# Optimization experiments

Hardware: AMD Instinct MI355X
Metric: run time of the kernel (lower is better)

## Reference

```python
import jax, jax.numpy as jnp
import numpy as np

TAU = 0.6  # BGK relaxation time (>= 0.5 per __post_init__ stability check)
# D2Q9 lattice: velocities, weights, opposite-direction indices
E = np.array([[0, 0], [1, 0], [0, 1], [-1, 0], [0, -1],
              [1, 1], [-1, 1], [-1, -1], [1, -1]], dtype=np.int32)
W = np.array([4.0 / 9] + [1.0 / 9] * 4 + [1.0 / 36] * 4, dtype=np.float32)
OPP = np.array([0, 3, 4, 1, 2, 7, 8, 5, 6], dtype=np.int32)


def setup_inputs() -> dict:
    key = jax.random.key(0)
    k1, k2, k3 = jax.random.split(key, 3)
    nx, ny = 2048, 2048
    f = jax.random.uniform(k1, (nx, ny, 9), dtype=jnp.float32)  # positive populations
    rho = jnp.sum(f, axis=-1)                                    # consistent density
    u = 0.05 * jax.random.normal(k2, (nx, ny, 2), dtype=jnp.float32)  # low-Ma velocity
    obstacle_mask = jax.random.uniform(k3, (nx, ny)) < 0.01      # sparse solid cells
    return {"f": f, "rho": rho, "u": u, "obstacle_mask": obstacle_mask}


def _equilibrium(rho, u):
    # feq_i = w_i * rho * (1 + 3 e.u + 4.5 (e.u)^2 - 1.5 u.u)
    e = jnp.asarray(E, jnp.float32)
    w = jnp.asarray(W)
    eu = jnp.einsum('xyd,qd->xyq', u, e)              # [nx, ny, 9]
    usq = jnp.sum(u * u, axis=-1, keepdims=True)       # [nx, ny, 1]
    return w * rho[..., None] * (1.0 + 3.0 * eu + 4.5 * eu * eu - 1.5 * usq)


def reference(f, rho, u, obstacle_mask):
    # --- collide (BGK) ---
    feq = _equilibrium(rho, u)
    f_star = f - (f - feq) / TAU
    # --- stream: roll each direction by its lattice velocity (lattice not shifted) ---
    f_new = jnp.stack(
        [jnp.roll(f_star[..., i], shift=(int(E[i, 0]), int(E[i, 1])), axis=(0, 1))
         for i in range(9)],
        axis=-1,
    )
    # --- obstacle bounce-back: solid cells reflect post-collision populations ---
    f_bb = f_star[..., jnp.asarray(OPP)]
    f_new = jnp.where(obstacle_mask[..., None], f_bb, f_new)
    # --- lift macro fields from post-stream distributions ---
    rho_new = jnp.sum(f_new, axis=-1)
    e = jnp.asarray(E, jnp.float32)
    u_new = jnp.einsum('xyq,qd->xyd', f_new, e) / rho_new[..., None]
    # pack (f_new [..9], rho_new [..1], u_new [..2]) -> [nx, ny, 12]
    return jnp.concatenate([f_new, rho_new[..., None], u_new], axis=-1)
```

## Files before the change

### kernel.cpp

```cpp
#include <hip/hip_runtime.h>


#define NX 2048
#define NY 2048
#define WRAP 2047
#define TR 8
#define TC 64
#define NT 512
#define HR (TR + 2)
#define HC (TC + 2)
#define HCELLS (HR * HC)
#define HELEMS (HCELLS * 9)
#define CACHEF (HCELLS * 4)
#define FP_ITERS 12
#define STAGE_WORDS (NT * 13)

typedef float floatx4 __attribute__((ext_vector_type(4)));

__global__ __launch_bounds__(NT) void lbm_step_kernel(
    const float* __restrict__ f,
    const float* __restrict__ rho,
    const float* __restrict__ u,
    const int*   __restrict__ mask,
    float*       __restrict__ out)
{
    __shared__ float lds[HELEMS + CACHEF];
    floatx4* cache = reinterpret_cast<floatx4*>(lds + HELEMS);

    const int tid = threadIdx.x;
    const int y0 = blockIdx.x * TC;
    const int x0 = blockIdx.y * TR;
    const float INV_TAU = 1.0f / 0.6f;

    const float2* __restrict__ u2 = reinterpret_cast<const float2*>(u);

    float fpre[FP_ITERS];
    #pragma unroll
    for (int it = 0; it < FP_ITERS; ++it) {
        const int k = tid + it * NT;
        if (k < HELEMS) {
            const unsigned cell = (unsigned)k / 9u;
            const int i  = k - (int)cell * 9;
            const unsigned hr = cell / (unsigned)HC;
            const int hc = (int)cell - (int)hr * HC;
            const int xr = (x0 - 1 + (int)hr) & WRAP;
            const int yc = (y0 - 1 + hc) & WRAP;
            const int g  = xr * NY + yc;
            fpre[it] = f[(size_t)g * 9 + i];
        }
    }

    const int r = tid >> 6;
    const int c = tid & 63;
    const int cidx = (x0 + r) * NY + (y0 + c);
    const int m = mask[cidx];

    for (int k = tid; k < HCELLS; k += NT) {
        const unsigned hr = (unsigned)k / (unsigned)HC;
        const int hc = k - (int)hr * HC;
        const int xr = (x0 - 1 + (int)hr) & WRAP;
        const int yc = (y0 - 1 + hc) & WRAP;
        const int g  = xr * NY + yc;
        const float  rn = rho[g];
        const float2 uv = u2[g];
        const float usq = uv.x * uv.x + uv.y * uv.y;
        floatx4 v;
        v.x = rn - 1.5f * rn * usq;
        v.y = 3.0f * rn * uv.x;
        v.z = 3.0f * rn * uv.y;
        v.w = __builtin_amdgcn_rcpf(rn + rn);
        cache[k] = v;
    }
    __syncthreads();

    #pragma unroll
    for (int it = 0; it < FP_ITERS; ++it) {
        const int k = tid + it * NT;
        if (k < HELEMS) {
            const unsigned cell = (unsigned)k / 9u;
            const int i  = k - (int)cell * 9;
            const floatx4 v = cache[cell];
            const float exf = (float)((int)((0x20919u >> (2 * i)) & 3u) - 1);
            const float eyf = (float)((int)((0x2865u  >> (2 * i)) & 3u) - 1);
            const float wi  = (i == 0) ? (4.0f / 9.0f)
                                       : ((i < 5) ? (1.0f / 9.0f) : (1.0f / 36.0f));
            const float t   = v.y * exf + v.z * eyf;
            const float feq = wi * (v.x + t + t * t * v.w);
            const float fi  = fpre[it];
            lds[k] = fi - (fi - feq) * INV_TAU;
        }
    }
    __syncthreads();

    const int ex9[9]  = {0, 1, 0, -1, 0, 1, -1, -1, 1};
    const int ey9[9]  = {0, 0, 1, 0, -1, 1, 1, -1, -1};
    const int opp9[9] = {0, 3, 4, 1, 2, 7, 8, 5, 6};

    float fn[9];
    #pragma unroll
    for (int i = 0; i < 9; ++i) {
        const int lsrc = (r + 1 - ex9[i]) * HC + (c + 1 - ey9[i]);
        fn[i] = lds[lsrc * 9 + i];
    }
    if (m) {
        const int lc = ((r + 1) * HC + (c + 1)) * 9;
        #pragma unroll
        for (int i = 0; i < 9; ++i) fn[i] = lds[lc + opp9[i]];
    }

    const float rhon = fn[0] + fn[1] + fn[2] + fn[3] + fn[4]
                     + fn[5] + fn[6] + fn[7] + fn[8];
    const float irho = __builtin_amdgcn_rcpf(rhon);
    const float uxn = (fn[1] - fn[3] + fn[5] - fn[6] - fn[7] + fn[8]) * irho;
    const float uyn = (fn[2] - fn[4] + fn[5] + fn[6] - fn[7] - fn[8]) * irho;

    __syncthreads();

    {
        const int b = tid * 13;
        #pragma unroll
        for (int i = 0; i < 9; ++i) lds[b + i] = fn[i];
        lds[b + 9]  = rhon;
        lds[b + 10] = uxn;
        lds[b + 11] = uyn;
    }
    __syncthreads();

    #pragma unroll
    for (int it = 0; it < 3; ++it) {
        const int k4 = tid + it * NT;
        const unsigned r2  = (unsigned)k4 / 192u;
        const int      rem = k4 - (int)r2 * 192;
        const unsigned cc  = (unsigned)rem / 3u;
        const int      q   = rem - (int)cc * 3;
        const int lbase = (int)r2 * (TC * 13) + (int)cc * 13 + q * 4;
        floatx4 v;
        v.x = lds[lbase + 0];
        v.y = lds[lbase + 1];
        v.z = lds[lbase + 2];
        v.w = lds[lbase + 3];
        const size_t obase = ((size_t)(x0 + (int)r2) * NY + y0) * 12 + (size_t)rem * 4;
        __builtin_nontemporal_store(v, reinterpret_cast<floatx4*>(out + obase));
    }
}

extern "C" void kernel_launch(void* const* d_in, const int* in_sizes, int n_in,
                              void* d_out, int out_size, void* d_ws, size_t ws_size,
                              hipStream_t stream) {
    const float* f    = (const float*)d_in[0];
    const float* rho  = (const float*)d_in[1];
    const float* u    = (const float*)d_in[2];
    const int*   mask = (const int*)d_in[3];
    float* out = (float*)d_out;

    dim3 block(NT, 1, 1);
    dim3 grid(NY / TC, NX / TR, 1);
    lbm_step_kernel<<<grid, block, 0, stream>>>(f, rho, u, mask, out);
}
```

Baseline: 349.4 us.

## Vectorize halo loads with row-contiguous LDS layout and per-cell collision

Reorganizes the LDS tile so each halo row stores its 64 interior cells contiguously, followed by the two wrap-around edge cells. Interior rows can then be loaded from global memory with 16-byte vector loads instead of scalar per-element gathers. Collision moves from per-element to per-cell, computing all nine equilibria from one rho/u read with shared subexpressions, and the separate rho/u cache array is dropped. Launch bounds now request 8 waves per EU. The cost is more register pressure per thread and special-case column indexing for the edge cells.

```diff
diff --git a/kernel.cpp b/kernel.cpp
--- a/kernel.cpp
+++ b/kernel.cpp
@@ -7,105 +7,136 @@
 #define TR 8
 #define TC 64
 #define NT 512
-#define HR (TR + 2)
-#define HC (TC + 2)
-#define HCELLS (HR * HC)
-#define HELEMS (HCELLS * 9)
-#define CACHEF (HCELLS * 4)
-#define FP_ITERS 12
-#define STAGE_WORDS (NT * 13)
+#define HCELLS 660
+#define RS 608
+#define LDSWORDS 6656
 
 typedef float floatx4 __attribute__((ext_vector_type(4)));
 
-__global__ __launch_bounds__(NT) void lbm_step_kernel(
+__global__ __launch_bounds__(NT, 8) void lbm_step_kernel(
     const float* __restrict__ f,
     const float* __restrict__ rho,
     const float* __restrict__ u,
     const int*   __restrict__ mask,
     float*       __restrict__ out)
 {
-    __shared__ float lds[HELEMS + CACHEF];
-    floatx4* cache = reinterpret_cast<floatx4*>(lds + HELEMS);
+    __shared__ __align__(16) float buf[LDSWORDS];
 
     const int tid = threadIdx.x;
     const int y0 = blockIdx.x * TC;
     const int x0 = blockIdx.y * TR;
-    const float INV_TAU = 1.0f / 0.6f;
 
     const float2* __restrict__ u2 = reinterpret_cast<const float2*>(u);
 
-    float fpre[FP_ITERS];
+    floatx4 bulkv[3];
+    int bulkdst[3] = {-1, -1, -1};
     #pragma unroll
-    for (int it = 0; it < FP_ITERS; ++it) {
+    for (int it = 0; it < 3; ++it) {
+        const int k4 = tid + it * NT;
+        if (k4 < 1440) {
+            const int row  = (unsigned)k4 / 144u;
+            const int col4 = k4 - row * 144;
+            const int xr   = (x0 - 1 + row) & WRAP;
+            const int srcf = (xr * NY + y0) * 9 + col4 * 4;
+            bulkv[it]   = *reinterpret_cast<const floatx4*>(f + srcf);
+            bulkdst[it] = row * RS + col4 * 4;
+        }
+    }
+    float edgev = 0.0f; int edgedst = -1;
+    if (tid < 180) {
+        const int side = tid >= 90;
+        const int er   = side ? tid - 90 : tid;
+        const int rowE = (unsigned)er / 9u;
+        const int i    = er - rowE * 9;
+        const int xr   = (x0 - 1 + rowE) & WRAP;
+        const int yc   = side ? ((y0 + TC) & WRAP) : ((y0 - 1) & WRAP);
+        edgev   = f[(xr * NY + yc) * 9 + i];
+        edgedst = rowE * RS + (side ? 585 : 576) + i;
+    }
+    float rr[2]; float2 uu[2]; int cbase[2] = {-1, -1};
+    #pragma unroll
+    for (int it = 0; it < 2; ++it) {
         const int k = tid + it * NT;
-        if (k < HELEMS) {
-            const unsigned cell = (unsigned)k / 9u;
-            const int i  = k - (int)cell * 9;
-            const unsigned hr = cell / (unsigned)HC;
-            const int hc = (int)cell - (int)hr * HC;
-            const int xr = (x0 - 1 + (int)hr) & WRAP;
+        if (k < HCELLS) {
+            const int hr = (unsigned)k / 66u;
+            const int hc = k - hr * 66;
+            const int xr = (x0 - 1 + hr) & WRAP;
             const int yc = (y0 - 1 + hc) & WRAP;
             const int g  = xr * NY + yc;
-            fpre[it] = f[(size_t)g * 9 + i];
+            rr[it] = rho[g];
+            uu[it] = u2[g];
+            cbase[it] = hr * RS + (hc == 0 ? 576 : (hc == 65 ? 585 : (hc - 1) * 9));
         }
     }
-
     const int r = tid >> 6;
     const int c = tid & 63;
-    const int cidx = (x0 + r) * NY + (y0 + c);
-    const int m = mask[cidx];
+    const int m = mask[(x0 + r) * NY + (y0 + c)];
 
-    for (int k = tid; k < HCELLS; k += NT) {
-        const unsigned hr = (unsigned)k / (unsigned)HC;
-        const int hc = k - (int)hr * HC;
-        const int xr = (x0 - 1 + (int)hr) & WRAP;
-        const int yc = (y0 - 1 + hc) & WRAP;
-        const int g  = xr * NY + yc;
-        const float  rn = rho[g];
-        const float2 uv = u2[g];
-        const float usq = uv.x * uv.x + uv.y * uv.y;
-        floatx4 v;
-        v.x = rn - 1.5f * rn * usq;
-        v.y = 3.0f * rn * uv.x;
-        v.z = 3.0f * rn * uv.y;
-        v.w = __builtin_amdgcn_rcpf(rn + rn);
-        cache[k] = v;
-    }
+    #pragma unroll
+    for (int it = 0; it < 3; ++it)
+        if (bulkdst[it] >= 0)
+            *reinterpret_cast<floatx4*>(&buf[bulkdst[it]]) = bulkv[it];
+    if (edgedst >= 0) buf[edgedst] = edgev;
     __syncthreads();
 
+    const float ITAU = 1.0f / 0.6f;
+    const float OMT  = 1.0f - ITAU;
     #pragma unroll
-    for (int it = 0; it < FP_ITERS; ++it) {
-        const int k = tid + it * NT;
-        if (k < HELEMS) {
-            const unsigned cell = (unsigned)k / 9u;
-            const int i  = k - (int)cell * 9;
-            const floatx4 v = cache[cell];
-            const float exf = (float)((int)((0x20919u >> (2 * i)) & 3u) - 1);
-            const float eyf = (float)((int)((0x2865u  >> (2 * i)) & 3u) - 1);
-            const float wi  = (i == 0) ? (4.0f / 9.0f)
-                                       : ((i < 5) ? (1.0f / 9.0f) : (1.0f / 36.0f));
-            const float t   = v.y * exf + v.z * eyf;
-            const float feq = wi * (v.x + t + t * t * v.w);
-            const float fi  = fpre[it];
-            lds[k] = fi - (fi - feq) * INV_TAU;
+    for (int it = 0; it < 2; ++it) {
+        if (cbase[it] >= 0) {
+            const int b0 = cbase[it];
+            float fi[9];
+            #pragma unroll
+            for (int i = 0; i < 9; ++i) fi[i] = buf[b0 + i];
+            const float rn = rr[it];
+            const float ux = uu[it].x, uy = uu[it].y;
+            const float C  = 1.0f - 1.5f * (ux * ux + uy * uy);
+            const float a  = 3.0f * ux, b = 3.0f * uy;
+            const float p  = a + b, q = a - b;
+            const float ha = 0.5f * a * a, hb = 0.5f * b * b;
+            const float hp = 0.5f * p * p, hq = 0.5f * q * q;
+            const float Pm = rn * (4.0f / 9.0f);
+            const float Ps = rn * (1.0f / 9.0f);
+            const float Pd = rn * (1.0f / 36.0f);
+            float feq[9];
+            feq[0] = Pm * C;
+            feq[1] = Ps * (C + a + ha);
+            feq[2] = Ps * (C + b + hb);
+            feq[3] = Ps * (C - a + ha);
+            feq[4] = Ps * (C - b + hb);
+            feq[5] = Pd * (C + p + hp);
+            feq[6] = Pd * (C - q + hq);
+            feq[7] = Pd * (C - p + hp);
+            feq[8] = Pd * (C + q + hq);
+            #pragma unroll
+            for (int i = 0; i < 9; ++i)
+                buf[b0 + i] = fmaf(feq[i], ITAU, OMT * fi[i]);
         }
     }
     __syncthreads();
 
-    const int ex9[9]  = {0, 1, 0, -1, 0, 1, -1, -1, 1};
-    const int ey9[9]  = {0, 0, 1, 0, -1, 1, 1, -1, -1};
-    const int opp9[9] = {0, 3, 4, 1, 2, 7, 8, 5, 6};
+    const int colmid = c * 9;
+    const int colL   = (c == 0)  ? 576 : (c - 1) * 9;
+    const int colR   = (c == 63) ? 585 : (c + 1) * 9;
+    const int rA = r * RS;
+    const int rB = rA + RS;
+    const int rC = rB + RS;
 
     float fn[9];
-    #pragma unroll
-    for (int i = 0; i < 9; ++i) {
-        const int lsrc = (r + 1 - ex9[i]) * HC + (c + 1 - ey9[i]);
-        fn[i] = lds[lsrc * 9 + i];
-    }
+    fn[0] = buf[rB + colmid + 0];
+    fn[1] = buf[rA + colmid + 1];
+    fn[2] = buf[rB + colL   + 2];
+    fn[3] = buf[rC + colmid + 3];
+    fn[4] = buf[rB + colR   + 4];
+    fn[5] = buf[rA + colL   + 5];
+    fn[6] = buf[rC + colL   + 6];
+    fn[7] = buf[rC + colR   + 7];
+    fn[8] = buf[rA + colR   + 8];
     if (m) {
-        const int lc = ((r + 1) * HC + (c + 1)) * 9;
+        const int ob = rB + colmid;
+        const int opp9[9] = {0, 3, 4, 1, 2, 7, 8, 5, 6};
         #pragma unroll
-        for (int i = 0; i < 9; ++i) fn[i] = lds[lc + opp9[i]];
+        for (int i = 0; i < 9; ++i) fn[i] = buf[ob + opp9[i]];
     }
 
     const float rhon = fn[0] + fn[1] + fn[2] + fn[3] + fn[4]
@@ -117,12 +148,12 @@
     __syncthreads();
 
     {
-        const int b = tid * 13;
+        const int b0 = tid * 13;
         #pragma unroll
-        for (int i = 0; i < 9; ++i) lds[b + i] = fn[i];
-        lds[b + 9]  = rhon;
-        lds[b + 10] = uxn;
-        lds[b + 11] = uyn;
+        for (int i = 0; i < 9; ++i) buf[b0 + i] = fn[i];
+        buf[b0 + 9]  = rhon;
+        buf[b0 + 10] = uxn;
+        buf[b0 + 11] = uyn;
     }
     __syncthreads();
 
@@ -135,10 +166,10 @@
         const int      q   = rem - (int)cc * 3;
         const int lbase = (int)r2 * (TC * 13) + (int)cc * 13 + q * 4;
         floatx4 v;
-        v.x = lds[lbase + 0];
-        v.y = lds[lbase + 1];
-        v.z = lds[lbase + 2];
-        v.w = lds[lbase + 3];
+        v.x = buf[lbase + 0];
+        v.y = buf[lbase + 1];
+        v.z = buf[lbase + 2];
+        v.w = buf[lbase + 3];
         const size_t obase = ((size_t)(x0 + (int)r2) * NY + y0) * 12 + (size_t)rem * 4;
         __builtin_nontemporal_store(v, reinterpret_cast<floatx4*>(out + obase));
     }
```

New measurement: 349.0 us. Within noise of the previous version (-0.1%).
